# Performance work log

Measured on AMD Instinct MI355X. Metric: run time of the kernel, lower is better.

The kernel has to match this reference:

```python
import jax, jax.numpy as jnp
import numpy as np

B, K, S = 4096, 32, 6          # batch, n_neighbors, n_shifts
QD, H, NH = 512, 384, 6        # query_dim, hidden_dim, n_heads
HD = H // NH                   # head_dim
NR = 20                        # n_residue_types (table has NR+1 rows)
NBR_IN = S + S + 16 + 1 + 1    # neighbor_proj input dim = 30

def gelu(x):
    return jax.nn.gelu(x, approximate=False)

def setup_inputs():
    key = jax.random.key(0)
    ks = iter(jax.random.split(key, 64))
    def nrm(shape, scale=0.05):
        return jax.random.normal(next(ks), shape, dtype=jnp.float32) * scale
    inp = {}
    inp['query_encoding'] = jax.random.normal(next(ks), (B, QD), dtype=jnp.float32)
    inp['query_residue_code'] = jax.random.randint(next(ks), (B,), 0, NR + 1).astype(jnp.int32)
    inp['query_observed_shifts'] = jax.random.normal(next(ks), (B, S), dtype=jnp.float32)
    inp['query_shift_masks'] = (jax.random.uniform(next(ks), (B, S)) < 0.8).astype(jnp.float32)
    inp['retrieved_shifts'] = jax.random.normal(next(ks), (B, K, S), dtype=jnp.float32)
    inp['retrieved_shift_masks'] = jax.random.uniform(next(ks), (B, K, S)) < 0.8
    inp['retrieved_residue_codes'] = jax.random.randint(next(ks), (B, K), 0, NR + 1).astype(jnp.int32)
    inp['retrieved_distances'] = jax.random.uniform(next(ks), (B, K), dtype=jnp.float32)
    inp['retrieved_valid'] = jax.random.uniform(next(ks), (B, K)) < 0.9
    # parameters (buffers + weights). rc_table kept finite (no NaN rows sampled).
    inp['rc_table'] = nrm((NR + 1, S), 1.0)
    inp['W_qp'] = nrm((QD, H)); inp['b_qp'] = jnp.zeros((H,))
    inp['E_res'] = nrm((NR + 1, 16))
    inp['W_np'] = nrm((NBR_IN, H)); inp['b_np'] = jnp.zeros((H,))
    inp['W_aq'] = nrm((H, H)); inp['b_aq'] = jnp.zeros((H,))
    inp['W_ak'] = nrm((H, H)); inp['b_ak'] = jnp.zeros((H,))
    inp['W_av'] = nrm((H, H)); inp['b_av'] = jnp.zeros((H,))
    inp['W_ss1'] = nrm((2 * S, H // 2)); inp['b_ss1'] = jnp.zeros((H // 2,))
    inp['W_ss2'] = nrm((H // 2, NH)); inp['b_ss2'] = jnp.zeros((NH,))
    inp['W_cp1'] = nrm((H, H)); inp['b_cp1'] = jnp.zeros((H,))
    inp['W_cp2'] = nrm((H, H)); inp['b_cp2'] = jnp.zeros((H,))
    inp['W_sw1'] = nrm((H, H)); inp['b_sw1'] = jnp.zeros((H,))
    inp['W_sw2'] = nrm((H, S)); inp['b_sw2'] = jnp.zeros((S,))
    inp['E_trust'] = nrm((NR + 1, 32))
    inp['W_tq'] = nrm((QD, H)); inp['b_tq'] = jnp.zeros((H,))
    inp['W_tc'] = nrm((H + 32 + 4, H)); inp['b_tc'] = jnp.zeros((H,))
    inp['W_tp1'] = nrm((H + 4, H // 2)); inp['b_tp1'] = jnp.zeros((H // 2,))
    inp['W_tp2'] = nrm((H // 2, 1)); inp['b_tp2'] = jnp.zeros((1,))
    inp['shift_scale'] = jnp.ones((S,)); inp['fallback_shift'] = jnp.zeros((S,))
    inp['fallback_context'] = jnp.zeros((H,))
    return inp

def _forward(p):
    eps = 1e-8
    qcode = p['query_residue_code']; rcodes = p['retrieved_residue_codes']
    smask = p['retrieved_shift_masks']; valid = p['retrieved_valid']
    dist = p['retrieved_distances']; rc = p['rc_table']
    # --- RC correction: corrected = RC[query] + (shift - RC[retrieved]) ---
    qidx = jnp.clip(qcode, 0, rc.shape[0] - 1)
    ridx = jnp.clip(rcodes, 0, rc.shape[0] - 1)
    rc_q = rc[qidx][:, None, :]            # (B,1,S)
    rc_r = rc[ridx]                         # (B,K,S)
    corrected = rc_q + (p['retrieved_shifts'] - rc_r)
    rc_valid = (~jnp.isnan(rc_q)) & (~jnp.isnan(rc_r))
    corrected = jnp.where(rc_valid, corrected, p['retrieved_shifts'])
    shifts = jnp.where(smask, corrected, p['retrieved_shifts'])  # (B,K,S)
    any_valid = valid.any(axis=1)                                # (B,)
    same_type = (rcodes == qcode[:, None]).astype(jnp.float32)   # (B,K)
    # --- projections ---
    q = gelu(p['query_encoding'] @ p['W_qp'] + p['b_qp'])        # (B,H)
    res_emb = p['E_res'][rcodes]                                 # (B,K,16)
    nbr = jnp.concatenate([shifts, smask.astype(jnp.float32), res_emb,
                           dist[..., None], same_type[..., None]], axis=-1)
    kv = gelu(nbr @ p['W_np'] + p['b_np'])                       # (B,K,H)
    # --- multi-head cross attention (single query token) ---
    Qh = (q @ p['W_aq'] + p['b_aq']).reshape(B, NH, HD)
    Kh = (kv @ p['W_ak'] + p['b_ak']).reshape(B, K, NH, HD)
    Vh = (kv @ p['W_av'] + p['b_av']).reshape(B, K, NH, HD)
    scores = jnp.einsum('bhd,bkhd->bhk', Qh, Kh) * (HD ** -0.5)  # (B,NH,K)
    sdiff = jnp.concatenate([
        (p['query_observed_shifts'][:, None, :] - shifts) * p['query_shift_masks'][:, None, :],
        jnp.broadcast_to(p['query_shift_masks'][:, None, :], (B, K, S))], axis=-1)
    bias = gelu(sdiff @ p['W_ss1'] + p['b_ss1']) @ p['W_ss2'] + p['b_ss2']  # (B,K,NH)
    scores = scores + jnp.transpose(bias, (0, 2, 1))
    # if nothing valid, unmask slot 0 (matches torch all_masked fixup)
    valid_eff = valid | ((~any_valid)[:, None] & (jnp.arange(K) == 0)[None, :])
    scores = jnp.where(valid_eff[:, None, :], scores, -10000.0)
    w = jax.nn.softmax(scores, axis=-1)
    attn_out = jnp.einsum('bhk,bkhd->bhd', w, Vh).reshape(B, H)
    ctx = gelu(attn_out @ p['W_cp1'] + p['b_cp1']) @ p['W_cp2'] + p['b_cp2']
    ctx = jnp.where(any_valid[:, None], ctx, p['fallback_context'][None, :])
    # --- shift transfer ---
    swb = gelu(attn_out @ p['W_sw1'] + p['b_sw1']) @ p['W_sw2'] + p['b_sw2']  # (B,S)
    weights = dist[..., None] + same_type[..., None] * 0.5 + swb[:, None, :] * 0.1  # (B,K,S)
    valid_mask = valid[..., None] & smask
    weights = jnp.where(valid_mask, weights, -10000.0)
    weights = jax.nn.softmax(weights, axis=1)
    transferred = jnp.sum(weights * shifts, axis=1) * p['shift_scale']
    transferred = jnp.where(any_valid[:, None], transferred, p['fallback_shift'][None, :])
    # --- trust statistics (no grad in original) ---
    vm = valid_mask.astype(jnp.float32)
    cnt = vm.sum(axis=1)                                         # (B,S)
    cov = cnt / (K + eps)
    mean = (shifts * vm).sum(axis=1) / (cnt + eps)
    var = (((shifts - mean[:, None, :]) ** 2) * vm).sum(axis=1) / (cnt + eps)
    var_n = jnp.clip(jnp.log1p(var), 0.0, 5.0) / 5.0
    mdist = (dist[..., None] * vm).sum(axis=1) / (cnt + eps)
    stp = (same_type[..., None] * vm).sum(axis=1) / (cnt + eps)
    per_stats = jax.lax.stop_gradient(jnp.stack([cov, var_n, mdist, stp], axis=-1))  # (B,S,4)
    vf = valid.astype(jnp.float32)
    n_valid = vf.sum(axis=1, keepdims=True) / K
    n_same = (same_type * vf).sum(axis=1, keepdims=True) / K
    dmask = jnp.where(valid, dist, 0.0)
    gmean = dmask.sum(axis=1, keepdims=True) / (vf.sum(axis=1, keepdims=True) + eps)
    gmax = dmask.max(axis=1, keepdims=True)
    gstats = jax.lax.stop_gradient(jnp.concatenate([gmean, gmax, n_valid, n_same], axis=-1))  # (B,4)
    # --- trust head ---
    qre = p['E_trust'][qcode]                                    # (B,32)
    tq = gelu(p['query_encoding'] @ p['W_tq'] + p['b_tq'])
    tc = gelu(jnp.concatenate([tq, qre, gstats], axis=-1) @ p['W_tc'] + p['b_tc'])  # (B,H)
    tin = jnp.concatenate([jnp.broadcast_to(tc[:, None, :], (B, S, H)), per_stats], axis=-1)
    trust = jax.nn.sigmoid(gelu(tin @ p['W_tp1'] + p['b_tp1']) @ p['W_tp2'] + p['b_tp2'])[..., 0]
    return ctx, transferred, trust

def reference(query_encoding, query_residue_code, query_observed_shifts, query_shift_masks,
              retrieved_shifts, retrieved_shift_masks, retrieved_residue_codes,
              retrieved_distances, retrieved_valid, rc_table,
              W_qp, b_qp, E_res, W_np, b_np, W_aq, b_aq, W_ak, b_ak, W_av, b_av,
              W_ss1, b_ss1, W_ss2, b_ss2, W_cp1, b_cp1, W_cp2, b_cp2,
              W_sw1, b_sw1, W_sw2, b_sw2, E_trust, W_tq, b_tq, W_tc, b_tc,
              W_tp1, b_tp1, W_tp2, b_tp2, shift_scale, fallback_shift, fallback_context):
    return _forward(dict(locals()))
```

## Files before the change

### kernel.cpp

```cpp
#include <hip/hip_runtime.h>

typedef unsigned short u16;
typedef unsigned int u32;
typedef __attribute__((ext_vector_type(8))) short bf16x8;
typedef __attribute__((ext_vector_type(4))) float f32x4;

__device__ __forceinline__ float fs(float f) {
    return (f == f && fabsf(f) < 1e30f) ? f : 0.f;
}
__device__ __forceinline__ float fin(float v) {
    return (v == v && fabsf(v) < 1e30f) ? v : 555.0f;
}
__device__ __forceinline__ u16 f2b(float f) {
    union { float f; unsigned int i; } w; w.f = f;
    unsigned int r = w.i + 0x7FFFu + ((w.i >> 16) & 1u);
    return (u16)(r >> 16);
}
__device__ __forceinline__ float b2f(u16 b) {
    union { unsigned int i; float f; } w; w.i = ((unsigned int)b) << 16;
    return w.f;
}
__device__ __forceinline__ float gelu_f(float x) {
    return 0.5f * x * (1.0f + erff(x * 0.70710678118654752440f));
}

__global__ void fill_kernel(float* __restrict__ out, int n, float val) {
    int i = blockIdx.x * 256 + threadIdx.x;
    if (i < n) out[i] = val;
}

__global__ void k_cvt(const float* __restrict__ in, u16* __restrict__ out, int n) {
    int i = blockIdx.x * 256 + threadIdx.x;
    if (i < n) out[i] = f2b(fs(in[i]));
}

__global__ void k_cvtT(const float* __restrict__ W, u16* __restrict__ WT,
                       int K, int N, int Kp, int total) {
    int id = blockIdx.x * 256 + threadIdx.x;
    if (id >= total) return;
    int n = id / Kp, k = id - n * Kp;
    WT[id] = (k < K) ? f2b(fs(W[(size_t)k * N + n])) : (u16)0;
}

__global__ void k_prep(const float* __restrict__ qobs, const float* __restrict__ qmask,
                       const float* __restrict__ rshift, const int* __restrict__ rsmask,
                       const int* __restrict__ qcode, const int* __restrict__ rcodes,
                       const float* __restrict__ rdist, const float* __restrict__ rc_table,
                       const float* __restrict__ E_res,
                       float* __restrict__ nbr, float* __restrict__ sdiff, int NBc)
{
    int gk = blockIdx.x * 256 + threadIdx.x;
    if (gk >= NBc) return;
    int b = gk >> 5;
    int qc = qcode[b], rc = rcodes[gk];
    int qi = min(max(qc, 0), 20), ri = min(max(rc, 0), 20);
    float dist = fs(rdist[gk]);
// ... 6 lines not shown
        float rq = rc_table[qi * 6 + s];
        float rr = rc_table[ri * 6 + s];
        bool rcv = (rq == rq) && (rr == rr) && fabsf(rq) < 1e30f && fabsf(rr) < 1e30f;
        float sh = (m && rcv) ? (rq + rs - rr) : rs;
        nr[s] = sh;
        nr[6 + s] = m ? 1.f : 0.f;
        float qm = fs(qmask[b * 6 + s]);
        sd[s] = (fs(qobs[b * 6 + s]) - sh) * qm;
        sd[6 + s] = qm;
    }
    for (int j = 0; j < 16; j++) nr[12 + j] = fs(E_res[ri * 16 + j]);
    nr[28] = dist;
    nr[29] = same;
}

__global__ void k_statsS_w(const float* __restrict__ nbr, const int* __restrict__ rvalid,
                           float* __restrict__ pst, int BCc)
{
    int wid = (blockIdx.x * 256 + threadIdx.x) >> 6;
    int lane = threadIdx.x & 63;
    if (wid >= BCc * 3) return;
    int b = wid / 3, s2 = wid - b * 3;
    int s = s2 * 2 + (lane >> 5), k = lane & 31;
    const float* nr = nbr + (size_t)(b * 32 + k) * 30;
    float vf = (rvalid[b * 32 + k] != 0) ? 1.f : 0.f;
    float vm = vf * nr[6 + s];
    float shv = nr[s], dist = nr[28], same = nr[29];
    float cnt = vm, msum = shv * vm, mdist = dist * vm, mst = same * vm;
#pragma unroll
    for (int m = 1; m <= 16; m <<= 1) {
        cnt += __shfl_xor(cnt, m);
        msum += __shfl_xor(msum, m);
        mdist += __shfl_xor(mdist, m);
        mst += __shfl_xor(mst, m);
    }
    float inv = 1.f / (cnt + 1e-8f);
    float mean = msum * inv;
    float dv = shv - mean;
    float var = dv * dv * vm;
#pragma unroll
    for (int m = 1; m <= 16; m <<= 1) var += __shfl_xor(var, m);
    var *= inv;
    if (k == 0) {
        float* p = pst + (size_t)b * 24 + s * 4;
        p[0] = cnt * (1.f / 32.f);
        p[1] = fminf(fmaxf(log1pf(var), 0.f), 5.f) * 0.2f;
        p[2] = mdist * inv;
        p[3] = mst * inv;
    }
}

__global__ void k_statsG_w(const float* __restrict__ nbr, const int* __restrict__ rvalid,
                           float* __restrict__ gst, float* __restrict__ anyv, int BCc)
{
    int wid = (blockIdx.x * 256 + threadIdx.x) >> 6;
    int lane = threadIdx.x & 63;
    if (wid >= BCc) return;
    int b = wid, k = lane & 31;
    float svf = 0.f, sdm = 0.f, mdm = -1e30f, ssm = 0.f;
    if (lane < 32) {
        const float* nr = nbr + (size_t)(b * 32 + k) * 30;
        float vf = (rvalid[b * 32 + k] != 0) ? 1.f : 0.f;
        float dm = vf * nr[28];
        svf = vf; sdm = dm; mdm = dm; ssm = vf * nr[29];
    }
#pragma unroll
    for (int m = 1; m <= 32; m <<= 1) {
        svf += __shfl_xor(svf, m);
        sdm += __shfl_xor(sdm, m);
        mdm = fmaxf(mdm, __shfl_xor(mdm, m));
        ssm += __shfl_xor(ssm, m);
    }
    if (lane == 0) {
        float* g = gst + (size_t)b * 4;
        g[0] = sdm / (svf + 1e-8f);
        g[1] = mdm;
        g[2] = svf * (1.f / 32.f);
        g[3] = ssm * (1.f / 32.f);
        anyv[b] = (svf > 0.f) ? 1.f : 0.f;
    }
}

template <int ACT, bool OUTF, bool OUTB>
__device__ __forceinline__ void gemm_body(
    const u16* __restrict__ A, int lda,
    const u16* __restrict__ BT, int ldb,
    const float* __restrict__ bias, const float* __restrict__ bias1,
    float* __restrict__ Cf, u16* __restrict__ Cb, int ldc,
    int K, int m0, int n0)
{
    __shared__ u16 As[64 * 72];
    __shared__ u16 Bs[64 * 72];
    const int t = threadIdx.x;
    const int lane = t & 63, wave = t >> 6;
// ... 52 lines not shown
{
    gemm_body<ACT, OUTF, OUTB>(A, lda, BT, ldb, bias, nullptr, Cf, Cb, ldc, K,
                               blockIdx.y << 6, blockIdx.x << 6);
}

template <int ACT>
__global__ __launch_bounds__(256) void k_gemm_bb2(
    const u16* __restrict__ A, int lda, const u16* __restrict__ BT, int ldb,
    const float* __restrict__ bias0, const float* __restrict__ bias1,
    u16* __restrict__ Cb, int ldc, int K)
{
    gemm_body<ACT, false, true>(A, lda, BT, ldb, bias0, bias1, nullptr, Cb, ldc, K,
                                blockIdx.y << 6, blockIdx.x << 6);
}

__global__ __launch_bounds__(256) void k_qp_bb(
    const u16* __restrict__ Qhb, const u16* __restrict__ WakB, u16* __restrict__ Qpb)
{
    int hd = blockIdx.z;
    gemm_body<0, false, true>(Qhb + hd * 64, 384, WakB + hd * 64, 384, nullptr, nullptr,
                              nullptr, Qpb + hd * 384, 2304, 64,
                              blockIdx.y << 6, blockIdx.x << 6);
}

__global__ __launch_bounds__(256) void k_attnout_bb(
    const u16* __restrict__ vmsb, const u16* __restrict__ WavT,
    const float* __restrict__ bav, u16* __restrict__ attnb)
{
    int hd = blockIdx.x;
    gemm_body<0, false, true>(vmsb + hd * 384, 2304, WavT + (size_t)hd * 64 * 384, 384,
                              bav + hd * 64, nullptr, nullptr, attnb + hd * 64, 384, 384,
                              blockIdx.y << 6, 0);
}

__global__ __launch_bounds__(192) void k_mlpbias(
    const float* __restrict__ sdiff, const float* __restrict__ Wss1,
    const float* __restrict__ bss1, const float* __restrict__ Wss2,
    const float* __restrict__ bss2, float* __restrict__ bias_s)
{
    __shared__ float sdS[32 * 12];
    __shared__ float hidS[32 * 193];
    __shared__ float w2S[1152];
    const int b = blockIdx.x;
    const int t = threadIdx.x;
    for (int i = t; i < 384; i += 192) sdS[i] = sdiff[(size_t)b * 384 + i];
    for (int i = t; i < 1152; i += 192) w2S[i] = fs(Wss2[i]);
    __syncthreads();
    {
        float w[12];
#pragma unroll
        for (int j = 0; j < 12; j++) w[j] = fs(Wss1[j * 192 + t]);
        float b1 = fs(bss1[t]);
        for (int k = 0; k < 32; k++) {
            float acc = b1;
#pragma unroll
            for (int j = 0; j < 12; j++) acc += sdS[k * 12 + j] * w[j];
            hidS[k * 193 + t] = gelu_f(acc);
        }
    }
    __syncthreads();
    {
        int k = t / 6, s = t - k * 6;
        float acc = fs(bss2[s]);
        for (int n = 0; n < 192; n++) acc += hidS[k * 193 + n] * w2S[n * 6 + s];
        bias_s[(size_t)(b * 32 + k) * 6 + s] = acc;
    }
}

__global__ void k_qkb_w(const float* __restrict__ Qh, const float* __restrict__ bak,
                        float* __restrict__ qkb, int BCc)
{
    int wid = (blockIdx.x * 256 + threadIdx.x) >> 6;
    int lane = threadIdx.x & 63;
    if (wid >= BCc * 6) return;
    int b = wid / 6, h = wid - b * 6;
    float acc = Qh[(size_t)b * 384 + h * 64 + lane] * fs(bak[h * 64 + lane]);
#pragma unroll
    for (int m = 1; m <= 32; m <<= 1) acc += __shfl_xor(acc, m);
    if (lane == 0) qkb[b * 6 + h] = acc;
}

__global__ __launch_bounds__(384) void k_attnblk(
    const float* __restrict__ nbr, const u16* __restrict__ WnpT,
    const float* __restrict__ bnp, const u16* __restrict__ Qpb,
    const float* __restrict__ qkb, const float* __restrict__ bias_s,
    const int* __restrict__ rvalid, const float* __restrict__ anyv,
    u16* __restrict__ vmsb)
{
    __shared__ u16 kvsb[32 * 392];
    __shared__ u16 qSb[6 * 392];
    __shared__ float wsx[192];
// ... 89 lines not shown
            a2 += wsx[64 + k] * kvv;
            a3 += wsx[96 + k] * kvv;
            a4 += wsx[128 + k] * kvv;
            a5 += wsx[160 + k] * kvv;
        }
        u16* vp = vmsb + (size_t)b * 2304;
        vp[t] = f2b(a0);
        vp[384 + t] = f2b(a1);
        vp[768 + t] = f2b(a2);
        vp[1152 + t] = f2b(a3);
        vp[1536 + t] = f2b(a4);
        vp[1920 + t] = f2b(a5);
    }
}

__global__ void k_ctxout(const float* __restrict__ ctx, const float* __restrict__ anyv,
                         const float* __restrict__ fctx, float* __restrict__ out, int BCc)
{
    int id = blockIdx.x * 256 + threadIdx.x;
    if (id >= BCc * 384) return;
    int b = id / 384, c = id - b * 384;
    float v = (anyv[b] > 0.f) ? ctx[id] : fs(fctx[c]);
    out[id] = fin(v);
}

__global__ void k_xtc_b(const u16* __restrict__ qtqb, const int* __restrict__ qcode,
                        const float* __restrict__ Etr, const float* __restrict__ gst,
                        u16* __restrict__ Xb, int BCc)
{
    int id = blockIdx.x * 256 + threadIdx.x;
    if (id >= BCc * 448) return;
    int b = id / 448, c = id - b * 448;
    if (c < 384) { Xb[id] = qtqb[(size_t)b * 768 + 384 + c]; return; }
    float v;
    if (c < 416) v = fs(Etr[min(max(qcode[b], 0), 20) * 32 + (c - 384)]);
    else if (c < 420) v = gst[(size_t)b * 4 + (c - 416)];
    else v = 0.f;
    Xb[id] = f2b(v);
}

// ... 3 lines not shown
    int wid = (blockIdx.x * 256 + threadIdx.x) >> 6;
    int lane = threadIdx.x & 63;
    if (wid >= BCc * 6) return;
    int b = wid / 6, s = wid - b * 6;
    float acc = 0.f;
#pragma unroll
    for (int i = 0; i < 6; i++) {
        int n = lane + 64 * i;
        acc += b2f(hs1b[(size_t)b * 768 + 384 + n]) * fs(Wsw2[n * 6 + s]);
    }
#pragma unroll
    for (int m = 1; m <= 32; m <<= 1) acc += __shfl_xor(acc, m);
    if (lane == 0) swb[b * 6 + s] = acc + fs(bsw2[s]);
}

__global__ void k_transfer_w(const float* __restrict__ nbr, const int* __restrict__ rsmask,
                             const int* __restrict__ rvalid, const float* __restrict__ swb,
                             const float* __restrict__ anyv, const float* __restrict__ sscale,
                             const float* __restrict__ fshift, float* __restrict__ out, int BCc)
{
    int wid = (blockIdx.x * 256 + threadIdx.x) >> 6;
    int lane = threadIdx.x & 63;
    if (wid >= BCc * 3) return;
    int b = wid / 3, s2 = wid - b * 3;
    int s = s2 * 2 + (lane >> 5), k = lane & 31;
    if (anyv[b] <= 0.f) {
        if (k == 0) out[b * 6 + s] = fin(fs(fshift[s]));
        return;
    }
    int gk = b * 32 + k;
    const float* nr = nbr + (size_t)gk * 30;
    float wb = swb[b * 6 + s] * 0.1f;
    bool m = (rvalid[gk] != 0) && (rsmask[gk * 6 + s] != 0);
    float wv = m ? (nr[28] + nr[29] * 0.5f + wb) : -10000.f;
    float mx = wv;
#pragma unroll
    for (int mm = 1; mm <= 16; mm <<= 1) mx = fmaxf(mx, __shfl_xor(mx, mm));
    float e = expf(wv - mx);
    float num = e * nr[s], den = e;
#pragma unroll
    for (int mm = 1; mm <= 16; mm <<= 1) {
        num += __shfl_xor(num, mm);
        den += __shfl_xor(den, mm);
    }
    if (k == 0) out[b * 6 + s] = fin((num / den) * fs(sscale[s]));
}

__global__ void k_trust_w(const float* __restrict__ tcp, const float* __restrict__ pst,
                          const float* __restrict__ Wtp1, const float* __restrict__ Wtp2,
                          const float* __restrict__ btp2, float* __restrict__ out, int BCc)
{
    int wid = (blockIdx.x * 256 + threadIdx.x) >> 6;
    int lane = threadIdx.x & 63;
    if (wid >= BCc * 6) return;
    int b = wid / 6, s = wid - b * 6;
    const float* ps = pst + (size_t)b * 24 + s * 4;
    float p0 = ps[0], p1 = ps[1], p2 = ps[2], p3 = ps[3];
    float acc = 0.f;
#pragma unroll
    for (int i = 0; i < 3; i++) {
        int j = lane + 64 * i;
        float pre = tcp[(size_t)b * 192 + j];
        pre += p0 * fs(Wtp1[(size_t)384 * 192 + j]);
        pre += p1 * fs(Wtp1[(size_t)385 * 192 + j]);
        pre += p2 * fs(Wtp1[(size_t)386 * 192 + j]);
        pre += p3 * fs(Wtp1[(size_t)387 * 192 + j]);
        acc += gelu_f(pre) * fs(Wtp2[j]);
    }
#pragma unroll
    for (int m = 1; m <= 32; m <<= 1) acc += __shfl_xor(acc, m);
    if (lane == 0) {
        float tv = 1.f / (1.f + expf(-(acc + fs(btp2[0]))));
        out[b * 6 + s] = fin(tv);
    }
}

#define L1(total) <<<((total) + 255) / 256, 256, 0, stream>>>
#define LW(nwaves) <<<(((nwaves) * 64) + 255) / 256, 256, 0, stream>>>

extern "C" void kernel_launch(void* const* d_in, const int* in_sizes, int n_in,
                              void* d_out, int out_size, void* d_ws, size_t ws_size,
                              hipStream_t stream)
{
    float* out = (float*)d_out;

    static const int EXP[45] = {
        2097152, 4096, 24576, 24576, 786432, 786432, 131072, 131072, 131072, 126,
        196608, 384, 336, 11520, 384, 147456, 384, 147456, 384, 147456, 384,
// ... 48 lines not shown
    const float* i_Wtq   = (const float*)d_in[34];
    const float* i_btq   = (const float*)d_in[35];
    const float* i_Wtc   = (const float*)d_in[36];
    const float* i_btc   = (const float*)d_in[37];
    const float* i_Wtp1  = (const float*)d_in[38];
    const float* i_btp1  = (const float*)d_in[39];
    const float* i_Wtp2  = (const float*)d_in[40];
    const float* i_btp2  = (const float*)d_in[41];
    const float* i_sscale= (const float*)d_in[42];
    const float* i_fshift= (const float*)d_in[43];
    const float* i_fctx  = (const float*)d_in[44];

    auto layoutBytes = [](int bc) -> size_t {
        auto al = [](size_t x) { return (x + 255) & ~(size_t)255; };
        size_t off = 0;
        off += al(2097152ull * 2);
        off += al(393216ull * 2);
        off += al(147456ull * 2) * 4;
        off += al(294912ull * 2);
        off += al(172032ull * 2);
        off += al(73728ull * 2);
        off += al(12288ull * 2);
        size_t nb = (size_t)bc * 32;
        off += al(nb * 30 * 4) + al(nb * 12 * 4) + al(nb * 6 * 4);
        off += al((size_t)bc * 384 * 4) * 2;
        off += al((size_t)bc * 192 * 4);
        off += al((size_t)bc * 2304 * 2) * 2;
        off += al((size_t)bc * 768 * 2) * 2;
        off += al((size_t)bc * 384 * 2) * 3;
        off += al((size_t)bc * 448 * 2);
        off += al((size_t)bc * 6 * 4) * 2 + al((size_t)bc * 24 * 4)
             + al((size_t)bc * 4 * 4) + al((size_t)bc * 4);
        return off;
    };
    const int cand[7] = {4096, 2048, 1024, 512, 256, 128, 64};
    int BCc = 64;
    for (int i = 0; i < 7; i++) {
        if (layoutBytes(cand[i]) <= ws_size) { BCc = cand[i]; break; }
    }
    const int NBc = BCc * 32;

    char* wsb = (char*)d_ws;
    size_t off = 0;
    auto allocB = [&](size_t bytes) -> void* {
        void* p = (void*)(wsb + off);
        off = (off + bytes + 255) & ~(size_t)255;
        return p;
    };
    u16* qeb    = (u16*)allocB(2097152ull * 2);
    u16* WqtqT  = (u16*)allocB(393216ull * 2);
    u16* WaqT   = (u16*)allocB(147456ull * 2);
    u16* WakB   = (u16*)allocB(147456ull * 2);
    u16* WavT   = (u16*)allocB(147456ull * 2);
    u16* Wcp2T  = (u16*)allocB(147456ull * 2);
    u16* Whs1T  = (u16*)allocB(294912ull * 2);
    u16* WtcT   = (u16*)allocB(172032ull * 2);
    u16* Wtp1T  = (u16*)allocB(73728ull * 2);
    u16* WnpT   = (u16*)allocB(12288ull * 2);
    float* nbr   = (float*)allocB((size_t)NBc * 30 * 4);
    float* sdiff = (float*)allocB((size_t)NBc * 12 * 4);
    float* bias_s= (float*)allocB((size_t)NBc * 6 * 4);
    float* Qhf   = (float*)allocB((size_t)BCc * 384 * 4);
    float* ctxf  = (float*)allocB((size_t)BCc * 384 * 4);
    float* tcpf  = (float*)allocB((size_t)BCc * 192 * 4);
    u16*   Qpb   = (u16*)allocB((size_t)BCc * 2304 * 2);
    u16*   vmsb  = (u16*)allocB((size_t)BCc * 2304 * 2);
    u16*   qtqb  = (u16*)allocB((size_t)BCc * 768 * 2);
    u16*   hs1b  = (u16*)allocB((size_t)BCc * 768 * 2);
    u16*   Qhb   = (u16*)allocB((size_t)BCc * 384 * 2);
    u16*   attnb = (u16*)allocB((size_t)BCc * 384 * 2);
    u16*   tcb   = (u16*)allocB((size_t)BCc * 384 * 2);
    u16*   Xfb   = (u16*)allocB((size_t)BCc * 448 * 2);
    float* swbf  = (float*)allocB((size_t)BCc * 6 * 4);
    float* qkbf  = (float*)allocB((size_t)BCc * 6 * 4);
    float* pstf  = (float*)allocB((size_t)BCc * 24 * 4);
    float* gstf  = (float*)allocB((size_t)BCc * 4 * 4);
    float* anyf  = (float*)allocB((size_t)BCc * 4);

    if (off > ws_size) {
        fill_kernel L1(out_size)(out, out_size, 1000.0f);
        return;
    }

    k_cvt L1(2097152)(i_qe, qeb, 2097152);
    k_cvtT L1(196608)(i_Wqp, WqtqT, 512, 384, 512, 196608);
    k_cvtT L1(196608)(i_Wtq, WqtqT + 196608, 512, 384, 512, 196608);
    k_cvtT L1(147456)(i_Waq, WaqT, 384, 384, 384, 147456);
    k_cvt L1(147456)(i_Wak, WakB, 147456);
    k_cvtT L1(147456)(i_Wav, WavT, 384, 384, 384, 147456);
    k_cvtT L1(147456)(i_Wcp2, Wcp2T, 384, 384, 384, 147456);
    k_cvtT L1(147456)(i_Wcp1, Whs1T, 384, 384, 384, 147456);
    k_cvtT L1(147456)(i_Wsw1, Whs1T + 147456, 384, 384, 384, 147456);
    k_cvtT L1(172032)(i_Wtc, WtcT, 420, 384, 448, 172032);
    k_cvtT L1(73728)(i_Wtp1, Wtp1T, 384, 192, 384, 73728);
    k_cvtT L1(12288)(i_Wnp, WnpT, 30, 384, 32, 12288);

    for (int c = 0; c < 4096 / BCc; c++) {
        const size_t B0 = (size_t)c * BCc;
        const dim3 g6(6, BCc / 64), g3(3, BCc / 64), g12(12, BCc / 64);
        const dim3 gqp(6, BCc / 64, 6), gao(6, BCc / 64);
        k_prep L1(NBc)(i_qobs + B0 * 6, i_qmask + B0 * 6, i_rshift + B0 * 192,
                       i_rsmask + B0 * 192, i_qcode + B0, i_rcodes + B0 * 32,
                       i_rdist + B0 * 32, i_rc, i_Eres, nbr, sdiff, NBc);
        k_statsS_w LW(BCc * 3)(nbr, i_rvalid + B0 * 32, pstf, BCc);
        k_statsG_w LW(BCc)(nbr, i_rvalid + B0 * 32, gstf, anyf, BCc);
        k_mlpbias<<<BCc, 192, 0, stream>>>(sdiff, i_Wss1, i_bss1, i_Wss2, i_bss2, bias_s);
        k_gemm_bb2<1><<<g12, 256, 0, stream>>>(
            qeb + B0 * 512, 512, WqtqT, 512, i_bqp, i_btq, qtqb, 768, 512);
        k_gemm_bb<0, true, true><<<g6, 256, 0, stream>>>(
            qtqb, 768, WaqT, 384, i_baq, Qhf, Qhb, 384, 384);
        k_qp_bb<<<gqp, 256, 0, stream>>>(Qhb, WakB, Qpb);
        k_qkb_w LW(BCc * 6)(Qhf, i_bak, qkbf, BCc);
        k_attnblk<<<BCc, 384, 0, stream>>>(nbr, WnpT, i_bnp, Qpb, qkbf, bias_s,
                                           i_rvalid + B0 * 32, anyf, vmsb);
        k_attnout_bb<<<gao, 256, 0, stream>>>(vmsb, WavT, i_bav, attnb);
        k_gemm_bb2<1><<<g12, 256, 0, stream>>>(
            attnb, 384, Whs1T, 384, i_bcp1, i_bsw1, hs1b, 768, 384);
        k_gemm_bb<0, true, false><<<g6, 256, 0, stream>>>(
            hs1b, 768, Wcp2T, 384, i_bcp2, ctxf, nullptr, 384, 384);
        k_swb_w LW(BCc * 6)(hs1b, i_Wsw2, i_bsw2, swbf, BCc);
        k_ctxout L1(BCc * 384)(ctxf, anyf, i_fctx, out + B0 * 384, BCc);
        k_xtc_b L1(BCc * 448)(qtqb, i_qcode + B0, i_Etr, gstf, Xfb, BCc);
        k_gemm_bb<1, false, true><<<g6, 256, 0, stream>>>(
            Xfb, 448, WtcT, 448, i_btc, nullptr, tcb, 384, 448);
        k_gemm_bb<0, true, false><<<g3, 256, 0, stream>>>(
            tcb, 384, Wtp1T, 384, i_btp1, tcpf, nullptr, 192, 384);
        k_trust_w LW(BCc * 6)(tcpf, pstf, i_Wtp1, i_Wtp2, i_btp2,
                              out + (size_t)4096 * 390 + B0 * 6, BCc);
        k_transfer_w LW(BCc * 3)(nbr, i_rsmask + B0 * 192, i_rvalid + B0 * 32, swbf, anyf,
                                 i_sscale, i_fshift, out + (size_t)4096 * 384 + B0 * 6, BCc);
    }
}
```

Measured before the change: 442.0 us.

## Merge conversion and small kernels, fuse ctx epilogue, MFMA mlpbias

Combines the twelve weight/activation conversion launches into one kernel over a contiguous workspace. It also merges the two stats kernels and the trust/transfer tail kernels, and folds the ctx fallback selection into the final GEMM epilogue. The FP32 Qh output is dropped in favour of the bf16 copy. The qp GEMM now loads the A tile once and loops over N tiles, and the second layer of mlpbias uses MFMA with a bf16 hidden layer. The aim is to cut launch overhead and intermediate traffic, at some cost in precision from the bf16 qk bias and hidden activations.

```diff
diff --git a/kernel.cpp b/kernel.cpp
--- a/kernel.cpp
+++ b/kernel.cpp
@@ -29,17 +29,27 @@
     if (i < n) out[i] = val;
 }
 
-__global__ void k_cvt(const float* __restrict__ in, u16* __restrict__ out, int n) {
-    int i = blockIdx.x * 256 + threadIdx.x;
-    if (i < n) out[i] = f2b(fs(in[i]));
-}
-
-__global__ void k_cvtT(const float* __restrict__ W, u16* __restrict__ WT,
-                       int K, int N, int Kp, int total) {
+struct CvtSrcs { const float* p[13]; };
+
+__global__ void k_cvt_all(CvtSrcs sp, u16* __restrict__ w) {
     int id = blockIdx.x * 256 + threadIdx.x;
-    if (id >= total) return;
-    int n = id / Kp, k = id - n * Kp;
-    WT[id] = (k < K) ? f2b(fs(W[(size_t)k * N + n])) : (u16)0;
+    if (id >= 3634304) return;
+    if (id < 2097152) { w[id] = f2b(fs(sp.p[0][id])); return; }
+    if (id >= 2637824 && id < 2785280) { w[id] = f2b(fs(sp.p[4][id - 2637824])); return; }
+    const float* src; int local, K, N, Kp;
+    if (id < 2293760)      { src = sp.p[1];  local = id - 2097152; K = 512; N = 384; Kp = 512; }
+    else if (id < 2490368) { src = sp.p[2];  local = id - 2293760; K = 512; N = 384; Kp = 512; }
+    else if (id < 2637824) { src = sp.p[3];  local = id - 2490368; K = 384; N = 384; Kp = 384; }
+    else if (id < 2932736) { src = sp.p[5];  local = id - 2785280; K = 384; N = 384; Kp = 384; }
+    else if (id < 3080192) { src = sp.p[6];  local = id - 2932736; K = 384; N = 384; Kp = 384; }
+    else if (id < 3227648) { src = sp.p[7];  local = id - 3080192; K = 384; N = 384; Kp = 384; }
+    else if (id < 3375104) { src = sp.p[8];  local = id - 3227648; K = 384; N = 384; Kp = 384; }
+    else if (id < 3547136) { src = sp.p[9];  local = id - 3375104; K = 420; N = 384; Kp = 448; }
+    else if (id < 3620864) { src = sp.p[10]; local = id - 3547136; K = 384; N = 192; Kp = 384; }
+    else if (id < 3633152) { src = sp.p[11]; local = id - 3620864; K = 30;  N = 384; Kp = 32;  }
+    else                   { src = sp.p[12]; local = id - 3633152; K = 192; N = 6;   Kp = 192; }
+    int n = local / Kp, k = local - n * Kp;
+    w[id] = (k < K) ? f2b(fs(src[(size_t)k * N + n])) : (u16)0;
 }
 
 __global__ void k_prep(const float* __restrict__ qobs, const float* __restrict__ qmask,
@@ -76,70 +86,66 @@
     nr[29] = same;
 }
 
-__global__ void k_statsS_w(const float* __restrict__ nbr, const int* __restrict__ rvalid,
-                           float* __restrict__ pst, int BCc)
+__global__ void k_stats_w(const float* __restrict__ nbr, const int* __restrict__ rvalid,
+                          float* __restrict__ pst, float* __restrict__ gst,
+                          float* __restrict__ anyv, int BCc)
 {
     int wid = (blockIdx.x * 256 + threadIdx.x) >> 6;
     int lane = threadIdx.x & 63;
-    if (wid >= BCc * 3) return;
-    int b = wid / 3, s2 = wid - b * 3;
-    int s = s2 * 2 + (lane >> 5), k = lane & 31;
-    const float* nr = nbr + (size_t)(b * 32 + k) * 30;
-    float vf = (rvalid[b * 32 + k] != 0) ? 1.f : 0.f;
-    float vm = vf * nr[6 + s];
-    float shv = nr[s], dist = nr[28], same = nr[29];
-    float cnt = vm, msum = shv * vm, mdist = dist * vm, mst = same * vm;
-#pragma unroll
-    for (int m = 1; m <= 16; m <<= 1) {
-        cnt += __shfl_xor(cnt, m);
-        msum += __shfl_xor(msum, m);
-        mdist += __shfl_xor(mdist, m);
-        mst += __shfl_xor(mst, m);
-    }
-    float inv = 1.f / (cnt + 1e-8f);
-    float mean = msum * inv;
-    float dv = shv - mean;
-    float var = dv * dv * vm;
-#pragma unroll
-    for (int m = 1; m <= 16; m <<= 1) var += __shfl_xor(var, m);
-    var *= inv;
-    if (k == 0) {
-        float* p = pst + (size_t)b * 24 + s * 4;
-        p[0] = cnt * (1.f / 32.f);
-        p[1] = fminf(fmaxf(log1pf(var), 0.f), 5.f) * 0.2f;
-        p[2] = mdist * inv;
-        p[3] = mst * inv;
-    }
-}
-
-__global__ void k_statsG_w(const float* __restrict__ nbr, const int* __restrict__ rvalid,
-                           float* __restrict__ gst, float* __restrict__ anyv, int BCc)
-{
-    int wid = (blockIdx.x * 256 + threadIdx.x) >> 6;
-    int lane = threadIdx.x & 63;
-    if (wid >= BCc) return;
-    int b = wid, k = lane & 31;
-    float svf = 0.f, sdm = 0.f, mdm = -1e30f, ssm = 0.f;
-    if (lane < 32) {
+    if (wid >= BCc * 4) return;
+    int b = wid >> 2, sub = wid & 3;
+    if (sub < 3) {
+        int s = sub * 2 + (lane >> 5), k = lane & 31;
         const float* nr = nbr + (size_t)(b * 32 + k) * 30;
         float vf = (rvalid[b * 32 + k] != 0) ? 1.f : 0.f;
-        float dm = vf * nr[28];
-        svf = vf; sdm = dm; mdm = dm; ssm = vf * nr[29];
-    }
-#pragma unroll
-    for (int m = 1; m <= 32; m <<= 1) {
-        svf += __shfl_xor(svf, m);
-        sdm += __shfl_xor(sdm, m);
-        mdm = fmaxf(mdm, __shfl_xor(mdm, m));
-        ssm += __shfl_xor(ssm, m);
-    }
-    if (lane == 0) {
-        float* g = gst + (size_t)b * 4;
-        g[0] = sdm / (svf + 1e-8f);
-        g[1] = mdm;
-        g[2] = svf * (1.f / 32.f);
-        g[3] = ssm * (1.f / 32.f);
-        anyv[b] = (svf > 0.f) ? 1.f : 0.f;
+        float vm = vf * nr[6 + s];
+        float shv = nr[s], dist = nr[28], same = nr[29];
+        float cnt = vm, msum = shv * vm, mdist = dist * vm, mst = same * vm;
+#pragma unroll
+        for (int m = 1; m <= 16; m <<= 1) {
+            cnt += __shfl_xor(cnt, m);
+            msum += __shfl_xor(msum, m);
+            mdist += __shfl_xor(mdist, m);
+            mst += __shfl_xor(mst, m);
+        }
+        float inv = 1.f / (cnt + 1e-8f);
+        float mean = msum * inv;
+        float dv = shv - mean;
+        float var = dv * dv * vm;
+#pragma unroll
+        for (int m = 1; m <= 16; m <<= 1) var += __shfl_xor(var, m);
+        var *= inv;
+        if (k == 0) {
+            float* p = pst + (size_t)b * 24 + s * 4;
+            p[0] = cnt * (1.f / 32.f);
+            p[1] = fminf(fmaxf(log1pf(var), 0.f), 5.f) * 0.2f;
+            p[2] = mdist * inv;
+            p[3] = mst * inv;
+        }
+    } else {
+        int k = lane & 31;
+        float svf = 0.f, sdm = 0.f, mdm = -1e30f, ssm = 0.f;
+        if (lane < 32) {
+            const float* nr = nbr + (size_t)(b * 32 + k) * 30;
+            float vf = (rvalid[b * 32 + k] != 0) ? 1.f : 0.f;
+            float dm = vf * nr[28];
+            svf = vf; sdm = dm; mdm = dm; ssm = vf * nr[29];
+        }
+#pragma unroll
+        for (int m = 1; m <= 32; m <<= 1) {
+            svf += __shfl_xor(svf, m);
+            sdm += __shfl_xor(sdm, m);
+            mdm = fmaxf(mdm, __shfl_xor(mdm, m));
+            ssm += __shfl_xor(ssm, m);
+        }
+        if (lane == 0) {
+            float* g = gst + (size_t)b * 4;
+            g[0] = sdm / (svf + 1e-8f);
+            g[1] = mdm;
+            g[2] = svf * (1.f / 32.f);
+            g[3] = ssm * (1.f / 32.f);
+            anyv[b] = (svf > 0.f) ? 1.f : 0.f;
+        }
     }
 }
 
@@ -222,13 +228,104 @@
                                 blockIdx.y << 6, blockIdx.x << 6);
 }
 
-__global__ __launch_bounds__(256) void k_qp_bb(
+__global__ __launch_bounds__(256) void k_gemm_ctx(
+    const u16* __restrict__ A, int lda, const u16* __restrict__ BT, int ldb,
+    const float* __restrict__ bias, const float* __restrict__ anyv,
+    const float* __restrict__ fctx, float* __restrict__ outp, int ldc, int K)
+{
+    __shared__ u16 As[64 * 72];
+    __shared__ u16 Bs[64 * 72];
+    const int t = threadIdx.x;
+    const int lane = t & 63, wave = t >> 6;
+    const int m0 = blockIdx.y << 6, n0 = blockIdx.x << 6;
+    const int wm = (wave & 1) << 5, wn = (wave >> 1) << 5;
+    const int frm = lane & 15, frq = lane >> 4;
+    const int r0 = t >> 3, c0 = (t & 7) << 3;
+    const f32x4 z = {0.f, 0.f, 0.f, 0.f};
+    f32x4 acc[2][2] = {{z, z}, {z, z}};
+    for (int k0 = 0; k0 < K; k0 += 64) {
+        *(bf16x8*)&As[r0 * 72 + c0]        = *(const bf16x8*)&A[(size_t)(m0 + r0) * lda + k0 + c0];
+        *(bf16x8*)&As[(r0 + 32) * 72 + c0] = *(const bf16x8*)&A[(size_t)(m0 + r0 + 32) * lda + k0 + c0];
+        *(bf16x8*)&Bs[r0 * 72 + c0]        = *(const bf16x8*)&BT[(size_t)(n0 + r0) * ldb + k0 + c0];
+        *(bf16x8*)&Bs[(r0 + 32) * 72 + c0] = *(const bf16x8*)&BT[(size_t)(n0 + r0 + 32) * ldb + k0 + c0];
+        __syncthreads();
+#pragma unroll
+        for (int kk = 0; kk < 2; kk++) {
+            const int fo = (kk << 5) + (frq << 3);
+            bf16x8 a0 = *(const bf16x8*)&As[(wm + frm) * 72 + fo];
+            bf16x8 a1 = *(const bf16x8*)&As[(wm + 16 + frm) * 72 + fo];
+            bf16x8 b0 = *(const bf16x8*)&Bs[(wn + frm) * 72 + fo];
+            bf16x8 b1 = *(const bf16x8*)&Bs[(wn + 16 + frm) * 72 + fo];
+            acc[0][0] = __builtin_amdgcn_mfma_f32_16x16x32_bf16(a0, b0, acc[0][0], 0, 0, 0);
+            acc[0][1] = __builtin_amdgcn_mfma_f32_16x16x32_bf16(a0, b1, acc[0][1], 0, 0, 0);
+            acc[1][0] = __builtin_amdgcn_mfma_f32_16x16x32_bf16(a1, b0, acc[1][0], 0, 0, 0);
+            acc[1][1] = __builtin_amdgcn_mfma_f32_16x16x32_bf16(a1, b1, acc[1][1], 0, 0, 0);
+        }
+        __syncthreads();
+    }
+#pragma unroll
+    for (int mi = 0; mi < 2; mi++) {
+#pragma unroll
+        for (int ni = 0; ni < 2; ni++) {
+            int col = n0 + wn + (ni << 4) + frm;
+            float bv = fs(bias[col]);
+            float fv = fs(fctx[col]);
+#pragma unroll
+            for (int r = 0; r < 4; r++) {
+                int row = m0 + wm + (mi << 4) + (frq << 2) + r;
+                float v = acc[mi][ni][r] + bv;
+                v = (anyv[row] > 0.f) ? v : fv;
+                outp[(size_t)row * ldc + col] = fin(v);
+            }
+        }
+    }
+}
+
+__global__ __launch_bounds__(256) void k_qp_loop(
     const u16* __restrict__ Qhb, const u16* __restrict__ WakB, u16* __restrict__ Qpb)
 {
-    int hd = blockIdx.z;
-    gemm_body<0, false, true>(Qhb + hd * 64, 384, WakB + hd * 64, 384, nullptr, nullptr,
-                              nullptr, Qpb + hd * 384, 2304, 64,
-                              blockIdx.y << 6, blockIdx.x << 6);
+    __shared__ u16 As[64 * 72];
+    __shared__ u16 Bs[64 * 72];
+    const int t = threadIdx.x;
+    const int lane = t & 63, wave = t >> 6;
+    const int m0 = blockIdx.x << 6, hd = blockIdx.y;
+    const int wm = (wave & 1) << 5, wn = (wave >> 1) << 5;
+    const int frm = lane & 15, frq = lane >> 4;
+    const int r0 = t >> 3, c0 = (t & 7) << 3;
+    const f32x4 z = {0.f, 0.f, 0.f, 0.f};
+    *(bf16x8*)&As[r0 * 72 + c0]        = *(const bf16x8*)&Qhb[(size_t)(m0 + r0) * 384 + hd * 64 + c0];
+    *(bf16x8*)&As[(r0 + 32) * 72 + c0] = *(const bf16x8*)&Qhb[(size_t)(m0 + r0 + 32) * 384 + hd * 64 + c0];
+    for (int nt = 0; nt < 6; nt++) {
+        *(bf16x8*)&Bs[r0 * 72 + c0]        = *(const bf16x8*)&WakB[(size_t)(nt * 64 + r0) * 384 + hd * 64 + c0];
+        *(bf16x8*)&Bs[(r0 + 32) * 72 + c0] = *(const bf16x8*)&WakB[(size_t)(nt * 64 + r0 + 32) * 384 + hd * 64 + c0];
+        __syncthreads();
+        f32x4 acc[2][2] = {{z, z}, {z, z}};
+#pragma unroll
+        for (int kk = 0; kk < 2; kk++) {
+            const int fo = (kk << 5) + (frq << 3);
+            bf16x8 a0 = *(const bf16x8*)&As[(wm + frm) * 72 + fo];
+            bf16x8 a1 = *(const bf16x8*)&As[(wm + 16 + frm) * 72 + fo];
+            bf16x8 b0 = *(const bf16x8*)&Bs[(wn + frm) * 72 + fo];
+            bf16x8 b1 = *(const bf16x8*)&Bs[(wn + 16 + frm) * 72 + fo];
+            acc[0][0] = __builtin_amdgcn_mfma_f32_16x16x32_bf16(a0, b0, acc[0][0], 0, 0, 0);
+            acc[0][1] = __builtin_amdgcn_mfma_f32_16x16x32_bf16(a0, b1, acc[0][1], 0, 0, 0);
+            acc[1][0] = __builtin_amdgcn_mfma_f32_16x16x32_bf16(a1, b0, acc[1][0], 0, 0, 0);
+            acc[1][1] = __builtin_amdgcn_mfma_f32_16x16x32_bf16(a1, b1, acc[1][1], 0, 0, 0);
+        }
+#pragma unroll
+        for (int mi = 0; mi < 2; mi++) {
+#pragma unroll
+            for (int ni = 0; ni < 2; ni++) {
+                int col = nt * 64 + wn + (ni << 4) + frm;
+#pragma unroll
+                for (int r = 0; r < 4; r++) {
+                    int row = m0 + wm + (mi << 4) + (frq << 2) + r;
+                    Qpb[(size_t)row * 2304 + hd * 384 + col] = f2b(acc[mi][ni][r]);
+                }
+            }
+        }
+        __syncthreads();
+    }
 }
 
 __global__ __launch_bounds__(256) void k_attnout_bb(
@@ -243,16 +340,14 @@
 
 __global__ __launch_bounds__(192) void k_mlpbias(
     const float* __restrict__ sdiff, const float* __restrict__ Wss1,
-    const float* __restrict__ bss1, const float* __restrict__ Wss2,
+    const float* __restrict__ bss1, const u16* __restrict__ Wss2T,
     const float* __restrict__ bss2, float* __restrict__ bias_s)
 {
     __shared__ float sdS[32 * 12];
-    __shared__ float hidS[32 * 193];
-    __shared__ float w2S[1152];
+    __shared__ u16 hidSb[32 * 200];
     const int b = blockIdx.x;
     const int t = threadIdx.x;
     for (int i = t; i < 384; i += 192) sdS[i] = sdiff[(size_t)b * 384 + i];
-    for (int i = t; i < 1152; i += 192) w2S[i] = fs(Wss2[i]);
     __syncthreads();
     {
         float w[12];
@@ -263,26 +358,43 @@
             float acc = b1;
 #pragma unroll
             for (int j = 0; j < 12; j++) acc += sdS[k * 12 + j] * w[j];
-            hidS[k * 193 + t] = gelu_f(acc);
+            hidSb[k * 200 + t] = f2b(gelu_f(acc));
         }
     }
     __syncthreads();
-    {
-        int k = t / 6, s = t - k * 6;
-        float acc = fs(bss2[s]);
-        for (int n = 0; n < 192; n++) acc += hidS[k * 193 + n] * w2S[n * 6 + s];
-        bias_s[(size_t)(b * 32 + k) * 6 + s] = acc;
-    }
-}
-
-__global__ void k_qkb_w(const float* __restrict__ Qh, const float* __restrict__ bak,
+    if (t < 64) {
+        const int frm = t & 15, frq = t >> 4;
+        const f32x4 z = {0.f, 0.f, 0.f, 0.f};
+        f32x4 acc0 = z, acc1 = z;
+        const u16* bt = Wss2T + (frm < 6 ? frm : 0) * 192;
+#pragma unroll
+        for (int ks = 0; ks < 6; ks++) {
+            bf16x8 bf = *(const bf16x8*)&bt[ks * 32 + (frq << 3)];
+            bf16x8 a0 = *(const bf16x8*)&hidSb[frm * 200 + ks * 32 + (frq << 3)];
+            bf16x8 a1 = *(const bf16x8*)&hidSb[(16 + frm) * 200 + ks * 32 + (frq << 3)];
+            acc0 = __builtin_amdgcn_mfma_f32_16x16x32_bf16(a0, bf, acc0, 0, 0, 0);
+            acc1 = __builtin_amdgcn_mfma_f32_16x16x32_bf16(a1, bf, acc1, 0, 0, 0);
+        }
+        if (frm < 6) {
+            float bb = fs(bss2[frm]);
+#pragma unroll
+            for (int r = 0; r < 4; r++) {
+                int kk = (frq << 2) + r;
+                bias_s[(size_t)(b * 32 + kk) * 6 + frm] = acc0[r] + bb;
+                bias_s[(size_t)(b * 32 + kk + 16) * 6 + frm] = acc1[r] + bb;
+            }
+        }
+    }
+}
+
+__global__ void k_qkb_w(const u16* __restrict__ Qhb, const float* __restrict__ bak,
                         float* __restrict__ qkb, int BCc)
 {
     int wid = (blockIdx.x * 256 + threadIdx.x) >> 6;
     int lane = threadIdx.x & 63;
     if (wid >= BCc * 6) return;
     int b = wid / 6, h = wid - b * 6;
-    float acc = Qh[(size_t)b * 384 + h * 64 + lane] * fs(bak[h * 64 + lane]);
+    float acc = b2f(Qhb[(size_t)b * 384 + h * 64 + lane]) * fs(bak[h * 64 + lane]);
 #pragma unroll
     for (int m = 1; m <= 32; m <<= 1) acc += __shfl_xor(acc, m);
     if (lane == 0) qkb[b * 6 + h] = acc;
@@ -402,16 +514,6 @@
     }
 }
 
-__global__ void k_ctxout(const float* __restrict__ ctx, const float* __restrict__ anyv,
-                         const float* __restrict__ fctx, float* __restrict__ out, int BCc)
-{
-    int id = blockIdx.x * 256 + threadIdx.x;
-    if (id >= BCc * 384) return;
-    int b = id / 384, c = id - b * 384;
-    float v = (anyv[b] > 0.f) ? ctx[id] : fs(fctx[c]);
-    out[id] = fin(v);
-}
-
 __global__ void k_xtc_b(const u16* __restrict__ qtqb, const int* __restrict__ qcode,
                         const float* __restrict__ Etr, const float* __restrict__ gst,
                         u16* __restrict__ Xb, int BCc)
@@ -445,64 +547,62 @@
     if (lane == 0) swb[b * 6 + s] = acc + fs(bsw2[s]);
 }
 
-__global__ void k_transfer_w(const float* __restrict__ nbr, const int* __restrict__ rsmask,
-                             const int* __restrict__ rvalid, const float* __restrict__ swb,
-                             const float* __restrict__ anyv, const float* __restrict__ sscale,
-                             const float* __restrict__ fshift, float* __restrict__ out, int BCc)
+__global__ void k_tail_w(const float* __restrict__ tcp, const float* __restrict__ pst,
+                         const float* __restrict__ Wtp1, const float* __restrict__ Wtp2,
+                         const float* __restrict__ btp2, float* __restrict__ outT,
+                         const float* __restrict__ nbr, const int* __restrict__ rsmask,
+                         const int* __restrict__ rvalid, const float* __restrict__ swb,
+                         const float* __restrict__ anyv, const float* __restrict__ sscale,
+                         const float* __restrict__ fshift, float* __restrict__ outX, int BCc)
 {
     int wid = (blockIdx.x * 256 + threadIdx.x) >> 6;
     int lane = threadIdx.x & 63;
-    if (wid >= BCc * 3) return;
-    int b = wid / 3, s2 = wid - b * 3;
-    int s = s2 * 2 + (lane >> 5), k = lane & 31;
-    if (anyv[b] <= 0.f) {
-        if (k == 0) out[b * 6 + s] = fin(fs(fshift[s]));
-        return;
-    }
-    int gk = b * 32 + k;
-    const float* nr = nbr + (size_t)gk * 30;
-    float wb = swb[b * 6 + s] * 0.1f;
-    bool m = (rvalid[gk] != 0) && (rsmask[gk * 6 + s] != 0);
-    float wv = m ? (nr[28] + nr[29] * 0.5f + wb) : -10000.f;
-    float mx = wv;
-#pragma unroll
-    for (int mm = 1; mm <= 16; mm <<= 1) mx = fmaxf(mx, __shfl_xor(mx, mm));
-    float e = expf(wv - mx);
-    float num = e * nr[s], den = e;
-#pragma unroll
-    for (int mm = 1; mm <= 16; mm <<= 1) {
-        num += __shfl_xor(num, mm);
-        den += __shfl_xor(den, mm);
-    }
-    if (k == 0) out[b * 6 + s] = fin((num / den) * fs(sscale[s]));
-}
-
-__global__ void k_trust_w(const float* __restrict__ tcp, const float* __restrict__ pst,
-                          const float* __restrict__ Wtp1, const float* __restrict__ Wtp2,
-                          const float* __restrict__ btp2, float* __restrict__ out, int BCc)
-{
-    int wid = (blockIdx.x * 256 + threadIdx.x) >> 6;
-    int lane = threadIdx.x & 63;
-    if (wid >= BCc * 6) return;
-    int b = wid / 6, s = wid - b * 6;
-    const float* ps = pst + (size_t)b * 24 + s * 4;
-    float p0 = ps[0], p1 = ps[1], p2 = ps[2], p3 = ps[3];
-    float acc = 0.f;
-#pragma unroll
-    for (int i = 0; i < 3; i++) {
-        int j = lane + 64 * i;
-        float pre = tcp[(size_t)b * 192 + j];
-        pre += p0 * fs(Wtp1[(size_t)384 * 192 + j]);
-        pre += p1 * fs(Wtp1[(size_t)385 * 192 + j]);
-        pre += p2 * fs(Wtp1[(size_t)386 * 192 + j]);
-        pre += p3 * fs(Wtp1[(size_t)387 * 192 + j]);
-        acc += gelu_f(pre) * fs(Wtp2[j]);
-    }
-#pragma unroll
-    for (int m = 1; m <= 32; m <<= 1) acc += __shfl_xor(acc, m);
-    if (lane == 0) {
-        float tv = 1.f / (1.f + expf(-(acc + fs(btp2[0]))));
-        out[b * 6 + s] = fin(tv);
+    if (wid >= BCc * 9) return;
+    int b = wid / 9, sub = wid - b * 9;
+    if (sub < 6) {
+        int s = sub;
+        const float* ps = pst + (size_t)b * 24 + s * 4;
+        float p0 = ps[0], p1 = ps[1], p2 = ps[2], p3 = ps[3];
+        float acc = 0.f;
+#pragma unroll
+        for (int i = 0; i < 3; i++) {
+            int j = lane + 64 * i;
+            float pre = tcp[(size_t)b * 192 + j];
+            pre += p0 * fs(Wtp1[(size_t)384 * 192 + j]);
+            pre += p1 * fs(Wtp1[(size_t)385 * 192 + j]);
+            pre += p2 * fs(Wtp1[(size_t)386 * 192 + j]);
+            pre += p3 * fs(Wtp1[(size_t)387 * 192 + j]);
+            acc += gelu_f(pre) * fs(Wtp2[j]);
+        }
+#pragma unroll
+        for (int m = 1; m <= 32; m <<= 1) acc += __shfl_xor(acc, m);
+        if (lane == 0) {
+            float tv = 1.f / (1.f + expf(-(acc + fs(btp2[0]))));
+            outT[b * 6 + s] = fin(tv);
+        }
+    } else {
+        int s2 = sub - 6;
+        int s = s2 * 2 + (lane >> 5), k = lane & 31;
+        if (anyv[b] <= 0.f) {
+            if (k == 0) outX[b * 6 + s] = fin(fs(fshift[s]));
+            return;
+        }
+        int gk = b * 32 + k;
+        const float* nr = nbr + (size_t)gk * 30;
+        float wb = swb[b * 6 + s] * 0.1f;
+        bool m = (rvalid[gk] != 0) && (rsmask[gk * 6 + s] != 0);
+        float wv = m ? (nr[28] + nr[29] * 0.5f + wb) : -10000.f;
+        float mx = wv;
+#pragma unroll
+        for (int mm = 1; mm <= 16; mm <<= 1) mx = fmaxf(mx, __shfl_xor(mx, mm));
+        float e = expf(wv - mx);
+        float num = e * nr[s], den = e;
+#pragma unroll
+        for (int mm = 1; mm <= 16; mm <<= 1) {
+            num += __shfl_xor(num, mm);
+            den += __shfl_xor(den, mm);
+        }
+        if (k == 0) outX[b * 6 + s] = fin((num / den) * fs(sscale[s]));
     }
 }
 
@@ -581,16 +681,9 @@
     auto layoutBytes = [](int bc) -> size_t {
         auto al = [](size_t x) { return (x + 255) & ~(size_t)255; };
         size_t off = 0;
-        off += al(2097152ull * 2);
-        off += al(393216ull * 2);
-        off += al(147456ull * 2) * 4;
-        off += al(294912ull * 2);
-        off += al(172032ull * 2);
-        off += al(73728ull * 2);
-        off += al(12288ull * 2);
+        off += al(3634304ull * 2);
         size_t nb = (size_t)bc * 32;
         off += al(nb * 30 * 4) + al(nb * 12 * 4) + al(nb * 6 * 4);
-        off += al((size_t)bc * 384 * 4) * 2;
         off += al((size_t)bc * 192 * 4);
         off += al((size_t)bc * 2304 * 2) * 2;
         off += al((size_t)bc * 768 * 2) * 2;
@@ -614,21 +707,21 @@
         off = (off + bytes + 255) & ~(size_t)255;
         return p;
     };
-    u16* qeb    = (u16*)allocB(2097152ull * 2);
-    u16* WqtqT  = (u16*)allocB(393216ull * 2);
-    u16* WaqT   = (u16*)allocB(147456ull * 2);
-    u16* WakB   = (u16*)allocB(147456ull * 2);
-    u16* WavT   = (u16*)allocB(147456ull * 2);
-    u16* Wcp2T  = (u16*)allocB(147456ull * 2);
-    u16* Whs1T  = (u16*)allocB(294912ull * 2);
-    u16* WtcT   = (u16*)allocB(172032ull * 2);
-    u16* Wtp1T  = (u16*)allocB(73728ull * 2);
-    u16* WnpT   = (u16*)allocB(12288ull * 2);
+    u16* wsW = (u16*)allocB(3634304ull * 2);
+    u16* qeb   = wsW;
+    u16* WqtqT = wsW + 2097152;
+    u16* WaqT  = wsW + 2490368;
+    u16* WakB  = wsW + 2637824;
+    u16* WavT  = wsW + 2785280;
+    u16* Wcp2T = wsW + 2932736;
+    u16* Whs1T = wsW + 3080192;
+    u16* WtcT  = wsW + 3375104;
+    u16* Wtp1T = wsW + 3547136;
+    u16* WnpT  = wsW + 3620864;
+    u16* Wss2T = wsW + 3633152;
     float* nbr   = (float*)allocB((size_t)NBc * 30 * 4);
     float* sdiff = (float*)allocB((size_t)NBc * 12 * 4);
     float* bias_s= (float*)allocB((size_t)NBc * 6 * 4);
-    float* Qhf   = (float*)allocB((size_t)BCc * 384 * 4);
-    float* ctxf  = (float*)allocB((size_t)BCc * 384 * 4);
     float* tcpf  = (float*)allocB((size_t)BCc * 192 * 4);
     u16*   Qpb   = (u16*)allocB((size_t)BCc * 2304 * 2);
     u16*   vmsb  = (u16*)allocB((size_t)BCc * 2304 * 2);
@@ -649,52 +742,44 @@
         return;
     }
 
-    k_cvt L1(2097152)(i_qe, qeb, 2097152);
-    k_cvtT L1(196608)(i_Wqp, WqtqT, 512, 384, 512, 196608);
-    k_cvtT L1(196608)(i_Wtq, WqtqT + 196608, 512, 384, 512, 196608);
-    k_cvtT L1(147456)(i_Waq, WaqT, 384, 384, 384, 147456);
-    k_cvt L1(147456)(i_Wak, WakB, 147456);
-    k_cvtT L1(147456)(i_Wav, WavT, 384, 384, 384, 147456);
-    k_cvtT L1(147456)(i_Wcp2, Wcp2T, 384, 384, 384, 147456);
-    k_cvtT L1(147456)(i_Wcp1, Whs1T, 384, 384, 384, 147456);
-    k_cvtT L1(147456)(i_Wsw1, Whs1T + 147456, 384, 384, 384, 147456);
-    k_cvtT L1(172032)(i_Wtc, WtcT, 420, 384, 448, 172032);
-    k_cvtT L1(73728)(i_Wtp1, Wtp1T, 384, 192, 384, 73728);
-    k_cvtT L1(12288)(i_Wnp, WnpT, 30, 384, 32, 12288);
+    CvtSrcs sp;
+    sp.p[0] = i_qe;  sp.p[1] = i_Wqp;  sp.p[2] = i_Wtq;  sp.p[3] = i_Waq;
+    sp.p[4] = i_Wak; sp.p[5] = i_Wav;  sp.p[6] = i_Wcp2; sp.p[7] = i_Wcp1;
+    sp.p[8] = i_Wsw1; sp.p[9] = i_Wtc; sp.p[10] = i_Wtp1; sp.p[11] = i_Wnp;
+    sp.p[12] = i_Wss2;
+    k_cvt_all L1(3634304)(sp, wsW);
 
     for (int c = 0; c < 4096 / BCc; c++) {
         const size_t B0 = (size_t)c * BCc;
         const dim3 g6(6, BCc / 64), g3(3, BCc / 64), g12(12, BCc / 64);
-        const dim3 gqp(6, BCc / 64, 6), gao(6, BCc / 64);
+        const dim3 gqp(BCc / 64, 6), gao(6, BCc / 64);
         k_prep L1(NBc)(i_qobs + B0 * 6, i_qmask + B0 * 6, i_rshift + B0 * 192,
                        i_rsmask + B0 * 192, i_qcode + B0, i_rcodes + B0 * 32,
                        i_rdist + B0 * 32, i_rc, i_Eres, nbr, sdiff, NBc);
-        k_statsS_w LW(BCc * 3)(nbr, i_rvalid + B0 * 32, pstf, BCc);
-        k_statsG_w LW(BCc)(nbr, i_rvalid + B0 * 32, gstf, anyf, BCc);
-        k_mlpbias<<<BCc, 192, 0, stream>>>(sdiff, i_Wss1, i_bss1, i_Wss2, i_bss2, bias_s);
+        k_stats_w LW(BCc * 4)(nbr, i_rvalid + B0 * 32, pstf, gstf, anyf, BCc);
+        k_mlpbias<<<BCc, 192, 0, stream>>>(sdiff, i_Wss1, i_bss1, Wss2T, i_bss2, bias_s);
         k_gemm_bb2<1><<<g12, 256, 0, stream>>>(
             qeb + B0 * 512, 512, WqtqT, 512, i_bqp, i_btq, qtqb, 768, 512);
-        k_gemm_bb<0, true, true><<<g6, 256, 0, stream>>>(
-            qtqb, 768, WaqT, 384, i_baq, Qhf, Qhb, 384, 384);
-        k_qp_bb<<<gqp, 256, 0, stream>>>(Qhb, WakB, Qpb);
-        k_qkb_w LW(BCc * 6)(Qhf, i_bak, qkbf, BCc);
+        k_gemm_bb<0, false, true><<<g6, 256, 0, stream>>>(
+            qtqb, 768, WaqT, 384, i_baq, nullptr, Qhb, 384, 384);
+        k_qp_loop<<<gqp, 256, 0, stream>>>(Qhb, WakB, Qpb);
+        k_qkb_w LW(BCc * 6)(Qhb, i_bak, qkbf, BCc);
         k_attnblk<<<BCc, 384, 0, stream>>>(nbr, WnpT, i_bnp, Qpb, qkbf, bias_s,
                                            i_rvalid + B0 * 32, anyf, vmsb);
         k_attnout_bb<<<gao, 256, 0, stream>>>(vmsb, WavT, i_bav, attnb);
         k_gemm_bb2<1><<<g12, 256, 0, stream>>>(
             attnb, 384, Whs1T, 384, i_bcp1, i_bsw1, hs1b, 768, 384);
-        k_gemm_bb<0, true, false><<<g6, 256, 0, stream>>>(
-            hs1b, 768, Wcp2T, 384, i_bcp2, ctxf, nullptr, 384, 384);
+        k_gemm_ctx<<<g6, 256, 0, stream>>>(
+            hs1b, 768, Wcp2T, 384, i_bcp2, anyf, i_fctx, out + B0 * 384, 384, 384);
         k_swb_w LW(BCc * 6)(hs1b, i_Wsw2, i_bsw2, swbf, BCc);
-        k_ctxout L1(BCc * 384)(ctxf, anyf, i_fctx, out + B0 * 384, BCc);
         k_xtc_b L1(BCc * 448)(qtqb, i_qcode + B0, i_Etr, gstf, Xfb, BCc);
         k_gemm_bb<1, false, true><<<g6, 256, 0, stream>>>(
             Xfb, 448, WtcT, 448, i_btc, nullptr, tcb, 384, 448);
         k_gemm_bb<0, true, false><<<g3, 256, 0, stream>>>(
             tcb, 384, Wtp1T, 384, i_btp1, tcpf, nullptr, 192, 384);
-        k_trust_w LW(BCc * 6)(tcpf, pstf, i_Wtp1, i_Wtp2, i_btp2,
-                              out + (size_t)4096 * 390 + B0 * 6, BCc);
-        k_transfer_w LW(BCc * 3)(nbr, i_rsmask + B0 * 192, i_rvalid + B0 * 32, swbf, anyf,
-                                 i_sscale, i_fshift, out + (size_t)4096 * 384 + B0 * 6, BCc);
-    }
-}
+        k_tail_w LW(BCc * 9)(tcpf, pstf, i_Wtp1, i_Wtp2, i_btp2,
+                             out + (size_t)4096 * 390 + B0 * 6,
+                             nbr, i_rsmask + B0 * 192, i_rvalid + B0 * 32, swbf, anyf,
+                             i_sscale, i_fshift, out + (size_t)4096 * 384 + B0 * 6, BCc);
+    }
+}
```

Measured after the change: 393.5 us. 11.0% less time.
